# Performance work log

Hardware: AMD Instinct MI355X
Metric: run time of the kernel (lower is better)

Reference implementation:

```python
import jax, jax.numpy as jnp
import numpy as np

N = 50000          # total nodes across all graphs
F = 3              # num_features
T = 64             # num_thetas
S = 64             # bump_steps
B = 128            # number of graphs (batch.max()+1)
R = 1.0
SHARP = 500.0      # sigmoid sharpness from the original code


def setup_inputs() -> dict:
    key = jax.random.key(0)
    k1, k2, k3 = jax.random.split(key, 3)
    x = jax.random.normal(k1, (N, F), dtype=jnp.float32)
    # directions v: uniform-0.5, row-normalized as in __init__
    v = jax.random.uniform(k2, (F, T), dtype=jnp.float32) - 0.5
    v = v / jnp.sqrt(jnp.sum(v * v, axis=0, keepdims=True))
    lin = jnp.linspace(-R, R, S, dtype=jnp.float32)
    batch = jnp.sort(jax.random.randint(k3, (N,), 0, B, dtype=jnp.int32))
    return {"x": x, "v": v, "lin": lin, "batch": batch}


def reference(x, v, lin, batch):
    # nh: (N, T) heights of each node along each direction
    nh = x @ v
    # broadcast bump: (N, S, T) = sigmoid(500 * (lin - nh))
    ecc = jax.nn.sigmoid(SHARP * (lin[None, :, None] - nh[:, None, :]))
    # scatter-sum over nodes into per-graph bins -> (B, S, T)
    # equals torch.index_add(out, 1, batch, ecc).movedim(0, 1)
    ect = jax.ops.segment_sum(ecc, batch, num_segments=B)
    return ect
```

## Files before the change

kernel.cpp:

```cpp
#include <hip/hip_runtime.h>


#define WAVES   8
#define THREADS (WAVES * 64)
#define HR      66

__global__ void ect_bounds_kernel(const int* __restrict__ batch,
                                  int* __restrict__ S, int N, int B)
{
    const int n = blockIdx.x * blockDim.x + threadIdx.x;
    if (n > N) return;
    const int cur  = (n < N) ? batch[n] : B;
    const int prev = (n > 0) ? batch[n - 1] : -1;
    for (int b = prev + 1; b <= cur; ++b) S[b] = n;
}

__global__ __launch_bounds__(THREADS) void ect_hist_kernel(
    const float* __restrict__ x,
    const float* __restrict__ v,
    const int*  __restrict__ S,
    float* __restrict__ out)
{
    const float KSH   = 721.3475204444817f;
    const float KSTEP = 22.900032395062912f;

    __shared__ float hist[WAVES][HR * 64];
    __shared__ float stripsum[WAVES][64];

    {
        float4* hz = (float4*)&hist[0][0];
        const int nf4 = WAVES * HR * 64 / 4;
        for (int i = threadIdx.x; i < nf4; i += THREADS)
            hz[i] = make_float4(0.f, 0.f, 0.f, 0.f);
    }
    __syncthreads();

    const int b     = blockIdx.x;
    const int start = S[b];
    const int end   = S[b + 1];

    const int t = threadIdx.x & 63;
    const int w = threadIdx.x >> 6;

    const float v0 = v[t];
    const float v1 = v[64 + t];
    const float v2 = v[128 + t];

    float* H = &hist[w][0];

#pragma unroll 2
    for (int n = start + w; n < end; n += WAVES) {
        const int ns = __builtin_amdgcn_readfirstlane(n);
        const float x0 = x[ns * 3 + 0];
        const float x1 = x[ns * 3 + 1];
        const float x2 = x[ns * 3 + 2];
        const float nh   = x0 * v0 + x1 * v1 + x2 * v2;
        const float a    = KSH * nh;
        const float fpos = fmaf(nh, 31.5f, 31.5f);
        const float cf   = floorf(fpos + 0.5f);
        const int   c    = (int)cf;

        const float arg = fmaf(-KSTEP, cf, a + KSH);
        const float sig = __builtin_amdgcn_rcpf(1.0f + __builtin_amdgcn_exp2f(arg));

        const int   p1  = min(max(c, 0), 64);
        const int   p2  = (c < 0) ? 65 : min(c + 1, 65);
        const float q1  = (c < 0) ? 1.0f : ((c > 63) ? 0.0f : sig);
        const float q2  = ((unsigned)c <= 63u) ? (1.0f - sig) : 0.0f;

        const int i1 = p1 * 64 + t;
        const int i2 = p2 * 64 + t;
        const float h1 = H[i1];
        const float h2 = H[i2];
        H[i1] = h1 + q1;
        H[i2] = h2 + q2;
    }
    __syncthreads();

    float tot[8];
    float strip = 0.0f;
#pragma unroll
    for (int i = 0; i < 8; ++i) {
        const int s = w * 8 + i;
        float sum = 0.0f;
#pragma unroll
        for (int w2 = 0; w2 < WAVES; ++w2) sum += hist[w2][s * 64 + t];
        tot[i] = sum;
        strip += sum;
    }
    stripsum[w][t] = strip;
    __syncthreads();

    float running = 0.0f;
    for (int w2 = 0; w2 < w; ++w2) running += stripsum[w2][t];

    float* ob = out + (size_t)b * 4096;
#pragma unroll
    for (int i = 0; i < 8; ++i) {
        running += tot[i];
        ob[(w * 8 + i) * 64 + t] = running;
    }
}

extern "C" void kernel_launch(void* const* d_in, const int* in_sizes, int n_in,
                              void* d_out, int out_size, void* d_ws, size_t ws_size,
                              hipStream_t stream)
{
    const float* x     = (const float*)d_in[0];
    const float* v     = (const float*)d_in[1];
    const int*   batch = (const int*)d_in[3];
    float*       out   = (float*)d_out;

    const int N = in_sizes[0] / 3;
    const int S = in_sizes[2];
    const int B = out_size / (S * 64);

    int* Sb = (int*)d_ws;

    ect_bounds_kernel<<<(N + 256) / 256, 256, 0, stream>>>(batch, Sb, N, B);
    ect_hist_kernel<<<B, THREADS, 0, stream>>>(x, v, Sb, out);
}
```

Measured before the change: 79.37 us.

## Fuse segment-bounds search into histogram kernel and process two nodes per iteration

```diff
diff --git a/kernel.cpp b/kernel.cpp
--- a/kernel.cpp
+++ b/kernel.cpp
@@ -5,21 +5,12 @@
 #define THREADS (WAVES * 64)
 #define HR      66
 
-__global__ void ect_bounds_kernel(const int* __restrict__ batch,
-                                  int* __restrict__ S, int N, int B)
-{
-    const int n = blockIdx.x * blockDim.x + threadIdx.x;
-    if (n > N) return;
-    const int cur  = (n < N) ? batch[n] : B;
-    const int prev = (n > 0) ? batch[n - 1] : -1;
-    for (int b = prev + 1; b <= cur; ++b) S[b] = n;
-}
-
-__global__ __launch_bounds__(THREADS) void ect_hist_kernel(
+__global__ __launch_bounds__(THREADS) void ect_fused_kernel(
     const float* __restrict__ x,
     const float* __restrict__ v,
-    const int*  __restrict__ S,
-    float* __restrict__ out)
+    const int*  __restrict__ batch,
+    float* __restrict__ out,
+    int N, int B)
 {
     const float KSH   = 721.3475204444817f;
     const float KSTEP = 22.900032395062912f;
@@ -33,45 +24,91 @@
         for (int i = threadIdx.x; i < nf4; i += THREADS)
             hz[i] = make_float4(0.f, 0.f, 0.f, 0.f);
     }
+
+    const int b = blockIdx.x;
+
+    int lo1 = 0, hi1 = N, lo2 = 0, hi2 = N;
+    while ((lo1 < hi1) || (lo2 < hi2)) {
+        if (lo1 < hi1) { const int m = (lo1 + hi1) >> 1;
+                         if (batch[m] <  b) lo1 = m + 1; else hi1 = m; }
+        if (lo2 < hi2) { const int m = (lo2 + hi2) >> 1;
+                         if (batch[m] <= b) lo2 = m + 1; else hi2 = m; }
+    }
+    const int start = lo1, end = lo2;
+
     __syncthreads();
-
-    const int b     = blockIdx.x;
-    const int start = S[b];
-    const int end   = S[b + 1];
 
     const int t = threadIdx.x & 63;
     const int w = threadIdx.x >> 6;
 
-    const float v0 = v[t];
-    const float v1 = v[64 + t];
-    const float v2 = v[128 + t];
+    const float vc0 = v[t];
+    const float vc1 = v[64 + t];
+    const float vc2 = v[128 + t];
 
     float* H = &hist[w][0];
 
+    int n = start + w * 2;
 #pragma unroll 2
-    for (int n = start + w; n < end; n += WAVES) {
+    for (; n + 1 < end; n += 2 * WAVES) {
         const int ns = __builtin_amdgcn_readfirstlane(n);
-        const float x0 = x[ns * 3 + 0];
-        const float x1 = x[ns * 3 + 1];
-        const float x2 = x[ns * 3 + 2];
-        const float nh   = x0 * v0 + x1 * v1 + x2 * v2;
-        const float a    = KSH * nh;
-        const float fpos = fmaf(nh, 31.5f, 31.5f);
-        const float cf   = floorf(fpos + 0.5f);
-        const int   c    = (int)cf;
+        const float xa0 = x[ns * 3 + 0], xa1 = x[ns * 3 + 1], xa2 = x[ns * 3 + 2];
+        const float xb0 = x[ns * 3 + 3], xb1 = x[ns * 3 + 4], xb2 = x[ns * 3 + 5];
 
-        const float arg = fmaf(-KSTEP, cf, a + KSH);
-        const float sig = __builtin_amdgcn_rcpf(1.0f + __builtin_amdgcn_exp2f(arg));
+        const float nhA = xa0 * vc0 + xa1 * vc1 + xa2 * vc2;
+        const float nhB = xb0 * vc0 + xb1 * vc1 + xb2 * vc2;
 
-        const int   p1  = min(max(c, 0), 64);
-        const int   p2  = (c < 0) ? 65 : min(c + 1, 65);
-        const float q1  = (c < 0) ? 1.0f : ((c > 63) ? 0.0f : sig);
-        const float q2  = ((unsigned)c <= 63u) ? (1.0f - sig) : 0.0f;
+        const float cfA = floorf(fmaf(nhA, 31.5f, 32.0f));
+        const float cfB = floorf(fmaf(nhB, 31.5f, 32.0f));
+        const int   cA  = (int)cfA;
+        const int   cB  = (int)cfB;
 
-        const int i1 = p1 * 64 + t;
-        const int i2 = p2 * 64 + t;
-        const float h1 = H[i1];
-        const float h2 = H[i2];
+        const float argA = fmaf(-KSTEP, cfA, fmaf(KSH, nhA, KSH));
+        const float argB = fmaf(-KSTEP, cfB, fmaf(KSH, nhB, KSH));
+        const float sA = __builtin_amdgcn_rcpf(1.0f + __builtin_amdgcn_exp2f(argA));
+        const float sB = __builtin_amdgcn_rcpf(1.0f + __builtin_amdgcn_exp2f(argB));
+
+        const int   p1A = min(max(cA, 0), 64);
+        const int   p2A = (cA < 0) ? 65 : min(cA + 1, 65);
+        const float q1A = (cA < 0) ? 1.0f : ((cA > 63) ? 0.0f : sA);
+        const float q2A = ((unsigned)cA <= 63u) ? (1.0f - sA) : 0.0f;
+
+        const int   p1B = min(max(cB, 0), 64);
+        const int   p2B = (cB < 0) ? 65 : min(cB + 1, 65);
+        const float q1B = (cB < 0) ? 1.0f : ((cB > 63) ? 0.0f : sB);
+        const float q2B = ((unsigned)cB <= 63u) ? (1.0f - sB) : 0.0f;
+
+        const int iA1 = p1A * 64 + t, iA2 = p2A * 64 + t;
+        const int iB1 = p1B * 64 + t, iB2 = p2B * 64 + t;
+
+        const float hA1 = H[iA1], hA2 = H[iA2];
+        const float hB1 = H[iB1], hB2 = H[iB2];
+
+        const float wA1 = hA1 + q1A;
+        const float wA2 = hA2 + q2A;
+        float wB1 = hB1 + q1B;
+        float wB2 = hB2 + q2B;
+        if (iB1 == iA1) wB1 += q1A;
+        if (iB1 == iA2) wB1 += q2A;
+        if (iB2 == iA1) wB2 += q1A;
+        if (iB2 == iA2) wB2 += q2A;
+
+        H[iA1] = wA1; H[iA2] = wA2;
+        H[iB1] = wB1; H[iB2] = wB2;
+    }
+    if (n < end) {
+        const int ns = __builtin_amdgcn_readfirstlane(n);
+        const float x0 = x[ns * 3 + 0], x1 = x[ns * 3 + 1], x2 = x[ns * 3 + 2];
+        const float nh = x0 * vc0 + x1 * vc1 + x2 * vc2;
+        const float cf = floorf(fmaf(nh, 31.5f, 32.0f));
+        const int   c  = (int)cf;
+        const float arg = fmaf(-KSTEP, cf, fmaf(KSH, nh, KSH));
+        const float sg  = __builtin_amdgcn_rcpf(1.0f + __builtin_amdgcn_exp2f(arg));
+        const int   p1 = min(max(c, 0), 64);
+        const int   p2 = (c < 0) ? 65 : min(c + 1, 65);
+        const float q1 = (c < 0) ? 1.0f : ((c > 63) ? 0.0f : sg);
+        const float q2 = ((unsigned)c <= 63u) ? (1.0f - sg) : 0.0f;
+        const int i1 = p1 * 64 + t, i2 = p2 * 64 + t;
+        const float h1 = H[i1], h2 = H[i2];
         H[i1] = h1 + q1;
         H[i2] = h2 + q2;
     }
@@ -115,8 +152,5 @@
     const int S = in_sizes[2];
     const int B = out_size / (S * 64);
 
-    int* Sb = (int*)d_ws;
-
-    ect_bounds_kernel<<<(N + 256) / 256, 256, 0, stream>>>(batch, Sb, N, B);
-    ect_hist_kernel<<<B, THREADS, 0, stream>>>(x, v, Sb, out);
+    ect_fused_kernel<<<B, THREADS, 0, stream>>>(x, v, batch, out, N, B);
 }
```

Result: no change. 79.75 us (+0.5%).
